# Kernel optimization log

Measured on AMD Instinct MI355X. Metric: run time of the kernel, lower is better.

Reference implementation:

```python
import jax, jax.numpy as jnp
import numpy as np

S, B, D_IN, D_OUT, E, R = 2048, 8, 1024, 4096, 8, 16

def setup_inputs() -> dict:
    key = jax.random.key(0)
    ks = jax.random.split(key, 6)
    x = jax.random.normal(ks[0], (S, B, D_IN), dtype=jnp.float32)
    gate_w = jax.random.normal(ks[1], (E, D_IN), dtype=jnp.float32) * 0.01  # std=0.01 init
    gate_b = jnp.zeros((E,), dtype=jnp.float32)  # init_lambda = 0
    W = jax.random.normal(ks[2], (D_OUT, D_IN), dtype=jnp.float32) * 0.02
    bias = jax.random.normal(ks[3], (D_OUT,), dtype=jnp.float32) * 0.02
    lora_A = jax.random.normal(ks[4], (E, R, D_IN), dtype=jnp.float32) * 0.02
    lora_B = jax.random.normal(ks[5], (E, D_OUT, R), dtype=jnp.float32) * 0.02
    return {"x": x, "gate_w": gate_w, "gate_b": gate_b, "W": W, "bias": bias,
            "lora_A": lora_A, "lora_B": lora_B}

def reference(x, gate_w, gate_b, W, bias, lora_A, lora_B):
    # gate: Linear(hidden, E) applied tokenwise, then mean over seq dim (dim 0, batch_first=False)
    gates = jnp.einsum('sbd,ed->sbe', x, gate_w) + gate_b      # [S,B,E]
    gate_weights = gates.mean(axis=0)                           # [B,E]
    # per-expert LoRA delta (detached in the torch original)
    delta = jnp.einsum('eor,eri->eoi', lora_B, lora_A)          # [E,D_OUT,D_IN]
    delta = jax.lax.stop_gradient(delta)
    # per-sample merged weight: W + sum_e g[b,e] * delta[e]
    W_b = W[None] + jnp.einsum('be,eoi->boi', gate_weights, delta)  # [B,D_OUT,D_IN]
    # per-sample linear (equivalent to looping functional_call over samples)
    out = jnp.einsum('sbi,boi->sbo', x, W_b) + bias             # [S,B,D_OUT]
    return out
```

## Files before the change

### kernel.cpp

```cpp
#include <hip/hip_runtime.h>
#include <stdint.h>

typedef unsigned short u16;
typedef __bf16 bf16x8 __attribute__((ext_vector_type(8)));
typedef float  f32x4  __attribute__((ext_vector_type(4)));

#define SDIM 2048
#define BDIM 8
#define DIN  1024
#define DOUT 4096
#define EDIM 8
#define RDIM 16
#define KAUG 1152
#define MDIM (SDIM*BDIM)
#define SCH  32
#define NT2  18

__device__ __forceinline__ u16 f2bf(float f) {
    __bf16 h = (__bf16)f;
    return __builtin_bit_cast(u16, h);
}

__device__ __forceinline__ void gload16(const u16* g, u16* lds) {
    __builtin_amdgcn_global_load_lds(
        (const __attribute__((address_space(1))) void*)g,
        (__attribute__((address_space(3))) void*)lds, 16, 0, 0);
}

#define VMCNT(n)  asm volatile("s_waitcnt vmcnt(" #n ")" ::: "memory")
#define LGKM0()   asm volatile("s_waitcnt lgkmcnt(0)" ::: "memory")
#define BARF()    do { asm volatile("" ::: "memory");                \
                       __builtin_amdgcn_s_barrier();                 \
                       asm volatile("" ::: "memory"); } while (0)

__global__ __launch_bounds__(256) void k1_reduce_convert(
    const float* __restrict__ x, u16* __restrict__ Xb, float* __restrict__ P)
{
    const int b  = blockIdx.x;
    const int sc = blockIdx.y;
    const int i  = threadIdx.x * 4;
    float a0 = 0.f, a1 = 0.f, a2 = 0.f, a3 = 0.f;
    const int s0 = sc * (SDIM / SCH);
    for (int s = s0; s < s0 + (SDIM / SCH); ++s) {
        const float4 v = *reinterpret_cast<const float4*>(
            &x[((size_t)s * BDIM + b) * DIN + i]);
        a0 += v.x; a1 += v.y; a2 += v.z; a3 += v.w;
        ushort4 u{f2bf(v.x), f2bf(v.y), f2bf(v.z), f2bf(v.w)};
        *reinterpret_cast<ushort4*>(&Xb[((size_t)s * BDIM + b) * KAUG + i]) = u;
    }
    float4 p{a0, a1, a2, a3};
    *reinterpret_cast<float4*>(&P[((size_t)sc * BDIM + b) * DIN + i]) = p;
}

__global__ __launch_bounds__(256) void k2_gates(
    const float* __restrict__ P, const float* __restrict__ gw,
    const float* __restrict__ gb, float* __restrict__ g)
{
    const int e = blockIdx.x, b = blockIdx.y, t = threadIdx.x;
    float dot = 0.f;
    for (int i = t; i < DIN; i += 256) {
        float xs = 0.f;
        #pragma unroll
        for (int c = 0; c < SCH; ++c) xs += P[((size_t)c * BDIM + b) * DIN + i];
        dot += xs * gw[(size_t)e * DIN + i];
    }
    __shared__ float red[256];
    red[t] = dot;
    __syncthreads();
    #pragma unroll
    for (int off = 128; off > 0; off >>= 1) {
        if (t < off) red[t] += red[t + off];
        __syncthreads();
    }
    if (t == 0) g[b * EDIM + e] = red[0] * (1.0f / SDIM) + gb[e];
}

__global__ __launch_bounds__(256) void kw_build_waug(
    const float* __restrict__ W, const float* __restrict__ lb, u16* __restrict__ Waug)
{
    const int o = blockIdx.x, t = threadIdx.x;
    for (int i = t; i < DIN; i += 256)
        Waug[(size_t)o * KAUG + i] = f2bf(W[(size_t)o * DIN + i]);
    if (t < EDIM * RDIM) {
        const int e = t >> 4, r = t & 15;
        Waug[(size_t)o * KAUG + DIN + t] =
            f2bf(lb[((size_t)e * DOUT + o) * RDIM + r]);
    }
}

__global__ __launch_bounds__(256) void kl_convert(
    const float* __restrict__ la, u16* __restrict__ LAb)
{
    const int idx = blockIdx.x * 256 + threadIdx.x;
    if (idx < EDIM * RDIM * DIN) LAb[idx] = f2bf(la[idx]);
}

__global__ __launch_bounds__(256) void gemm_lora(
    const u16* __restrict__ A, const u16* __restrict__ B,
    const float* __restrict__ G, u16* __restrict__ Xb)
{
    __shared__ __align__(16) u16 As[128][64];
    __shared__ __align__(16) u16 Bs[128][64];

    const int tid  = threadIdx.x;
    const int lane = tid & 63;
    const int l15  = lane & 15;
    const int l4   = lane >> 4;
    const int sw   = lane & 7;
    const int wid  = tid >> 6;
    const int wr   = wid >> 1;
    const int wc   = wid & 1;
    const int m0 = blockIdx.y * 128;

    f32x4 acc[4][4] = {};

    for (int kt = 0; kt < DIN / 64; ++kt) {
        #pragma unroll
        for (int ii = 0; ii < 4; ++ii) {
            const int cix = ii * 256 + tid;
            const int row = cix >> 3, cl = cix & 7;
            const int kof = kt * 64 + ((cl ^ (row & 7)) << 3);
            gload16(A + (size_t)(m0 + row) * KAUG + kof, &As[0][0] + cix * 8);
            gload16(B + (size_t)row * DIN + kof, &Bs[0][0] + cix * 8);
        }
        __syncthreads();
        #pragma unroll
        for (int ks = 0; ks < 2; ++ks) {
            bf16x8 av[4], bv[4];
            #pragma unroll
            for (int mi = 0; mi < 4; ++mi)
                av[mi] = *reinterpret_cast<const bf16x8*>(
                    &As[wr * 64 + mi * 16 + l15][((ks * 4 + l4) ^ sw) << 3]);
            #pragma unroll
            for (int ni = 0; ni < 4; ++ni)
                bv[ni] = *reinterpret_cast<const bf16x8*>(
                    &Bs[wc * 64 + ni * 16 + l15][((ks * 4 + l4) ^ sw) << 3]);
            #pragma unroll
            for (int mi = 0; mi < 4; ++mi)
                #pragma unroll
                for (int ni = 0; ni < 4; ++ni)
                    acc[mi][ni] = __builtin_amdgcn_mfma_f32_16x16x32_bf16(
                        av[mi], bv[ni], acc[mi][ni], 0, 0, 0);
        }
        __syncthreads();
    }

    #pragma unroll
    for (int mi = 0; mi < 4; ++mi) {
        const int r0 = m0 + wr * 64 + mi * 16 + l4 * 4;
        #pragma unroll
        for (int ni = 0; ni < 4; ++ni) {
            const int col = wc * 64 + ni * 16 + l15;
            const int e   = col >> 4;
            #pragma unroll
            for (int r = 0; r < 4; ++r) {
                const int row = r0 + r;
                const float gv = G[((row & 7) << 3) + e];
                Xb[(size_t)row * KAUG + DIN + col] = f2bf(gv * acc[mi][ni][r]);
            }
        }
    }
}

__global__ __launch_bounds__(512) void gemm_main(
    const u16* __restrict__ A, const u16* __restrict__ Bm,
    float* __restrict__ C, const float* __restrict__ bias)
{
    __shared__ __align__(16) u16 As[2][2][128][64];
    __shared__ __align__(16) u16 Bs[2][2][128][64];

    const int tid  = threadIdx.x;
    const int lane = tid & 63;
    const int l15  = lane & 15;
    const int l4   = lane >> 4;
    const int sw   = lane & 7;
    const int wid  = tid >> 6;
    const int wm   = wid >> 2;
    const int wn   = wid & 3;
    const int bh   = wn >> 1;
    const int bl   = wn & 1;

    const int f   = blockIdx.x + blockIdx.y * gridDim.x;
    const int xcd = f & 7, k = f >> 3;
    const int gn  = xcd & 3, gm = xcd >> 2;
    const int n0  = (gn * 4 + (k & 3)) * 256;
    const int m0  = (gm * 32 + (k >> 2)) * 256;

    f32x4  acc[8][4] = {};
    bf16x8 aq[2][2], bv[4][2];

    auto stageA = [&](int t, int hf) {
        const int buf = t & 1;
        #pragma unroll
        for (int ii = 0; ii < 2; ++ii) {
            const int cix = ii * 512 + tid;
            const int row = cix >> 3, cl = cix & 7;
            const int kof = t * 64 + ((cl ^ (row & 7)) << 3);
            gload16(A + (size_t)(m0 + hf * 128 + row) * KAUG + kof,
                    &As[buf][hf][0][0] + cix * 8);
        }
    };
    auto stageB = [&](int t, int hf) {
        const int buf = t & 1;
        #pragma unroll
        for (int ii = 0; ii < 2; ++ii) {
            const int cix = ii * 512 + tid;
            const int row = cix >> 3, cl = cix & 7;
            const int kof = t * 64 + ((cl ^ (row & 7)) << 3);
            gload16(Bm + (size_t)(n0 + hf * 128 + row) * KAUG + kof,
                    &Bs[buf][hf][0][0] + cix * 8);
        }
    };

    #define RD_BV(BUF)                                                        \
        _Pragma("unroll") for (int nf = 0; nf < 4; ++nf)                      \
            _Pragma("unroll") for (int kk = 0; kk < 2; ++kk)                  \
                bv[nf][kk] = *reinterpret_cast<const bf16x8*>(                \
                    &Bs[BUF][bh][bl * 64 + nf * 16 + l15]                     \
                       [((kk * 4 + l4) ^ sw) << 3]);
    #define RD_AQ(BUF, Q)                                                     \
        _Pragma("unroll") for (int fr = 0; fr < 2; ++fr)                      \
            _Pragma("unroll") for (int kk = 0; kk < 2; ++kk)                  \
                aq[fr][kk] = *reinterpret_cast<const bf16x8*>(                \
                    &As[BUF][wm][(Q) * 32 + fr * 16 + l15]                    \
                       [((kk * 4 + l4) ^ sw) << 3]);
    #define MMA(Q)                                                            \
        do {                                                                  \
            __builtin_amdgcn_s_setprio(1);                                    \
            _Pragma("unroll") for (int kk = 0; kk < 2; ++kk)                  \
                _Pragma("unroll") for (int fr = 0; fr < 2; ++fr)              \
                    _Pragma("unroll") for (int nf = 0; nf < 4; ++nf)          \
                        acc[(Q) * 2 + fr][nf] =                               \
                            __builtin_amdgcn_mfma_f32_16x16x32_bf16(          \
                                aq[fr][kk], bv[nf][kk],                       \
                                acc[(Q) * 2 + fr][nf], 0, 0, 0);              \
            __builtin_amdgcn_s_setprio(0);                                    \
        } while (0)

    stageA(0, 0); stageA(0, 1); stageB(0, 0); stageB(0, 1);
    stageA(1, 0); stageA(1, 1); stageB(1, 0); stageB(1, 1);
    VMCNT(8);
    BARF();

    for (int j = 0; j < NT2; ++j) {
        const int buf = j & 1;
        RD_BV(buf);
        RD_AQ(buf, 0);
        if (j >= 1 && j + 1 < NT2) stageA(j + 1, 0);
        BARF();
        LGKM0();
        __builtin_amdgcn_sched_barrier(0);
        MMA(0);
        BARF();
        RD_AQ(buf, 1);
        if (j >= 1 && j + 1 < NT2) stageA(j + 1, 1);
        BARF();
        LGKM0();
        __builtin_amdgcn_sched_barrier(0);
        MMA(1);
        BARF();
        RD_AQ(buf, 2);
        if (j + 2 < NT2) stageB(j + 2, 0);
        BARF();
        LGKM0();
        __builtin_amdgcn_sched_barrier(0);
        MMA(2);
        BARF();
        RD_AQ(buf, 3);
        if (j + 2 < NT2) stageB(j + 2, 1);
        BARF();
        LGKM0();
        __builtin_amdgcn_sched_barrier(0);
        MMA(3);
        if (j <= NT2 - 3) { VMCNT(4); } else { VMCNT(0); }
        BARF();
    }
    #undef RD_BV
    #undef RD_AQ
    #undef MMA

    #pragma unroll
    for (int a = 0; a < 8; ++a) {
        const int row0 = m0 + wm * 128 + a * 16 + l4 * 4;
        #pragma unroll
        for (int nf = 0; nf < 4; ++nf) {
            const int col = n0 + wn * 64 + nf * 16 + l15;
            const float badd = bias[col];
            float* cp = C + (size_t)row0 * DOUT + col;
            #pragma unroll
            for (int q = 0; q < 4; ++q)
                cp[(size_t)q * DOUT] = acc[a][nf][q] + badd;
        }
    }
}

extern "C" void kernel_launch(void* const* d_in, const int* in_sizes, int n_in,
                              void* d_out, int out_size, void* d_ws, size_t ws_size,
                              hipStream_t stream)
{
    const float* x    = (const float*)d_in[0];
    const float* gw   = (const float*)d_in[1];
    const float* gb   = (const float*)d_in[2];
    const float* W    = (const float*)d_in[3];
    const float* bias = (const float*)d_in[4];
    const float* la   = (const float*)d_in[5];
    const float* lb   = (const float*)d_in[6];
    float* out = (float*)d_out;

    char* ws = (char*)d_ws;
    u16*   Xb   = (u16*)(ws);
    u16*   Waug = (u16*)(ws + 37748736);
    float* P    = (float*)(ws + 47185920);
    u16*   LAb  = (u16*)(ws + 48234496);
    float* G    = (float*)(ws + 48496640);

    k1_reduce_convert<<<dim3(BDIM, SCH), 256, 0, stream>>>(x, Xb, P);
    kw_build_waug<<<DOUT, 256, 0, stream>>>(W, lb, Waug);
    kl_convert<<<(EDIM * RDIM * DIN + 255) / 256, 256, 0, stream>>>(la, LAb);
    k2_gates<<<dim3(EDIM, BDIM), 256, 0, stream>>>(P, gw, gb, G);
    gemm_lora<<<dim3(1, MDIM / 128), 256, 0, stream>>>(Xb, LAb, G, Xb);
    gemm_main<<<dim3(DOUT / 256, MDIM / 256), 512, 0, stream>>>(
        Xb, Waug, out, bias);
}
```

Measured before the change: 249.0 us.

## Pre-swizzle weights into MFMA fragment layout and load B directly to registers

The augmented weight matrix is now built in a fragment-major layout, so each lane's 16-byte B operand for the 16x16x32 MFMA is one contiguous global load. The main GEMM drops the B shared-memory tile and reads B straight into two register banks that alternate between even and odd K tiles, which also halves the per-tile barrier count. The aim is to cut LDS traffic and synchronisation for B. In exchange every wave reads B from global/L2 with no reuse across the block, register pressure rises, and each tile ends with a full vmcnt(0) wait, leaving no prefetch depth beyond one tile.

```diff
diff --git a/kernel.cpp b/kernel.cpp
--- a/kernel.cpp
+++ b/kernel.cpp
@@ -15,6 +15,8 @@
 #define MDIM (SDIM*BDIM)
 #define SCH  32
 #define NT2  18
+#define NCB  (DOUT/16)
+#define NKC  (KAUG/8)
 
 __device__ __forceinline__ u16 f2bf(float f) {
     __bf16 h = (__bf16)f;
@@ -28,7 +30,6 @@
 }
 
 #define VMCNT(n)  asm volatile("s_waitcnt vmcnt(" #n ")" ::: "memory")
-#define LGKM0()   asm volatile("s_waitcnt lgkmcnt(0)" ::: "memory")
 #define BARF()    do { asm volatile("" ::: "memory");                \
                        __builtin_amdgcn_s_barrier();                 \
                        asm volatile("" ::: "memory"); } while (0)
@@ -75,16 +76,29 @@
     if (t == 0) g[b * EDIM + e] = red[0] * (1.0f / SDIM) + gb[e];
 }
 
-__global__ __launch_bounds__(256) void kw_build_waug(
-    const float* __restrict__ W, const float* __restrict__ lb, u16* __restrict__ Waug)
-{
-    const int o = blockIdx.x, t = threadIdx.x;
-    for (int i = t; i < DIN; i += 256)
-        Waug[(size_t)o * KAUG + i] = f2bf(W[(size_t)o * DIN + i]);
-    if (t < EDIM * RDIM) {
-        const int e = t >> 4, r = t & 15;
-        Waug[(size_t)o * KAUG + DIN + t] =
-            f2bf(lb[((size_t)e * DOUT + o) * RDIM + r]);
+__global__ __launch_bounds__(256) void kwf_build_waugf(
+    const float* __restrict__ W, const float* __restrict__ lb, u16* __restrict__ WF)
+{
+    const int cb = blockIdx.x, t = threadIdx.x;
+    const int ln = t & 15;
+    const int o  = cb * 16 + ln;
+    #pragma unroll
+    for (int bq = 0; bq < 9; ++bq) {
+        const int kc = (t >> 4) + 16 * bq;
+        u16 v[8];
+        if (kc < 128) {
+            #pragma unroll
+            for (int q = 0; q < 8; ++q)
+                v[q] = f2bf(W[(size_t)o * DIN + kc * 8 + q]);
+        } else {
+            const int e = (kc - 128) >> 1, rh = (kc - 128) & 1;
+            #pragma unroll
+            for (int q = 0; q < 8; ++q)
+                v[q] = f2bf(lb[((size_t)e * DOUT + o) * RDIM + rh * 8 + q]);
+        }
+        u16* dst = WF + (((size_t)cb * NKC + kc) * 16 + ln) * 8;
+        *reinterpret_cast<ushort4*>(dst)     = ushort4{v[0], v[1], v[2], v[3]};
+        *reinterpret_cast<ushort4*>(dst + 4) = ushort4{v[4], v[5], v[6], v[7]};
     }
 }
 
@@ -163,11 +177,10 @@
 }
 
 __global__ __launch_bounds__(512) void gemm_main(
-    const u16* __restrict__ A, const u16* __restrict__ Bm,
+    const u16* __restrict__ A, const u16* __restrict__ WF,
     float* __restrict__ C, const float* __restrict__ bias)
 {
     __shared__ __align__(16) u16 As[2][2][128][64];
-    __shared__ __align__(16) u16 Bs[2][2][128][64];
 
     const int tid  = threadIdx.x;
     const int lane = tid & 63;
@@ -177,17 +190,18 @@
     const int wid  = tid >> 6;
     const int wm   = wid >> 2;
     const int wn   = wid & 3;
-    const int bh   = wn >> 1;
-    const int bl   = wn & 1;
 
     const int f   = blockIdx.x + blockIdx.y * gridDim.x;
-    const int xcd = f & 7, k = f >> 3;
+    const int xcd = f & 7, kk_ = f >> 3;
     const int gn  = xcd & 3, gm = xcd >> 2;
-    const int n0  = (gn * 4 + (k & 3)) * 256;
-    const int m0  = (gm * 32 + (k >> 2)) * 256;
+    const int n0  = (gn * 4 + (kk_ & 3)) * 256;
+    const int m0  = (gm * 32 + (kk_ >> 2)) * 256;
+
+    const int cb0 = (n0 >> 4) + wn * 4;
 
     f32x4  acc[8][4] = {};
-    bf16x8 aq[2][2], bv[4][2];
+    bf16x8 aq[2][2];
+    bf16x8 bvE[4][2], bvO[4][2];
 
     auto stageA = [&](int t, int hf) {
         const int buf = t & 1;
@@ -200,31 +214,19 @@
                     &As[buf][hf][0][0] + cix * 8);
         }
     };
-    auto stageB = [&](int t, int hf) {
-        const int buf = t & 1;
-        #pragma unroll
-        for (int ii = 0; ii < 2; ++ii) {
-            const int cix = ii * 512 + tid;
-            const int row = cix >> 3, cl = cix & 7;
-            const int kof = t * 64 + ((cl ^ (row & 7)) << 3);
-            gload16(Bm + (size_t)(n0 + hf * 128 + row) * KAUG + kof,
-                    &Bs[buf][hf][0][0] + cix * 8);
-        }
-    };
-
-    #define RD_BV(BUF)                                                        \
+
+    #define BLOAD(T, KK, BANK)                                                \
         _Pragma("unroll") for (int nf = 0; nf < 4; ++nf)                      \
-            _Pragma("unroll") for (int kk = 0; kk < 2; ++kk)                  \
-                bv[nf][kk] = *reinterpret_cast<const bf16x8*>(                \
-                    &Bs[BUF][bh][bl * 64 + nf * 16 + l15]                     \
-                       [((kk * 4 + l4) ^ sw) << 3]);
+            BANK[nf][KK] = *reinterpret_cast<const bf16x8*>(                  \
+                WF + (((size_t)(cb0 + nf) * NKC + ((T) * 8 + (KK) * 4 + l4))  \
+                      * 16 + l15) * 8);
     #define RD_AQ(BUF, Q)                                                     \
         _Pragma("unroll") for (int fr = 0; fr < 2; ++fr)                      \
             _Pragma("unroll") for (int kk = 0; kk < 2; ++kk)                  \
                 aq[fr][kk] = *reinterpret_cast<const bf16x8*>(                \
                     &As[BUF][wm][(Q) * 32 + fr * 16 + l15]                    \
                        [((kk * 4 + l4) ^ sw) << 3]);
-    #define MMA(Q)                                                            \
+    #define MMA(Q, BANK)                                                      \
         do {                                                                  \
             __builtin_amdgcn_s_setprio(1);                                    \
             _Pragma("unroll") for (int kk = 0; kk < 2; ++kk)                  \
@@ -232,52 +234,44 @@
                     _Pragma("unroll") for (int nf = 0; nf < 4; ++nf)          \
                         acc[(Q) * 2 + fr][nf] =                               \
                             __builtin_amdgcn_mfma_f32_16x16x32_bf16(          \
-                                aq[fr][kk], bv[nf][kk],                       \
+                                aq[fr][kk], BANK[nf][kk],                     \
                                 acc[(Q) * 2 + fr][nf], 0, 0, 0);              \
             __builtin_amdgcn_s_setprio(0);                                    \
         } while (0)
 
-    stageA(0, 0); stageA(0, 1); stageB(0, 0); stageB(0, 1);
-    stageA(1, 0); stageA(1, 1); stageB(1, 0); stageB(1, 1);
-    VMCNT(8);
+    #define TILE(T, BVU, BVL)                                                 \
+    do {                                                                      \
+        const int buf_ = (T) & 1;                                             \
+                                             \
+        RD_AQ(buf_, 0);                                                       \
+        if ((T) + 1 < NT2) { stageA((T) + 1, 0); BLOAD((T) + 1, 0, BVL); }    \
+        MMA(0, BVU);                                                          \
+        RD_AQ(buf_, 1);                                                       \
+        MMA(1, BVU);                                                          \
+        BARF();                                                               \
+                                             \
+        RD_AQ(buf_, 2);                                                       \
+        if ((T) + 1 < NT2) { stageA((T) + 1, 1); BLOAD((T) + 1, 1, BVL); }    \
+        MMA(2, BVU);                                                          \
+        RD_AQ(buf_, 3);                                                       \
+        MMA(3, BVU);                                                          \
+        VMCNT(0);                                                             \
+        BARF();                                                               \
+    } while (0)
+
+    stageA(0, 0); stageA(0, 1);
+    BLOAD(0, 0, bvE); BLOAD(0, 1, bvE);
+    VMCNT(0);
     BARF();
 
-    for (int j = 0; j < NT2; ++j) {
-        const int buf = j & 1;
-        RD_BV(buf);
-        RD_AQ(buf, 0);
-        if (j >= 1 && j + 1 < NT2) stageA(j + 1, 0);
-        BARF();
-        LGKM0();
-        __builtin_amdgcn_sched_barrier(0);
-        MMA(0);
-        BARF();
-        RD_AQ(buf, 1);
-        if (j >= 1 && j + 1 < NT2) stageA(j + 1, 1);
-        BARF();
-        LGKM0();
-        __builtin_amdgcn_sched_barrier(0);
-        MMA(1);
-        BARF();
-        RD_AQ(buf, 2);
-        if (j + 2 < NT2) stageB(j + 2, 0);
-        BARF();
-        LGKM0();
-        __builtin_amdgcn_sched_barrier(0);
-        MMA(2);
-        BARF();
-        RD_AQ(buf, 3);
-        if (j + 2 < NT2) stageB(j + 2, 1);
-        BARF();
-        LGKM0();
-        __builtin_amdgcn_sched_barrier(0);
-        MMA(3);
-        if (j <= NT2 - 3) { VMCNT(4); } else { VMCNT(0); }
-        BARF();
-    }
-    #undef RD_BV
+    for (int jj = 0; jj < NT2; jj += 2) {
+        TILE(jj,     bvE, bvO);
+        TILE(jj + 1, bvO, bvE);
+    }
+    #undef TILE
+    #undef MMA
     #undef RD_AQ
-    #undef MMA
+    #undef BLOAD
 
     #pragma unroll
     for (int a = 0; a < 8; ++a) {
@@ -309,16 +303,16 @@
 
     char* ws = (char*)d_ws;
     u16*   Xb   = (u16*)(ws);
-    u16*   Waug = (u16*)(ws + 37748736);
+    u16*   WF   = (u16*)(ws + 37748736);
     float* P    = (float*)(ws + 47185920);
     u16*   LAb  = (u16*)(ws + 48234496);
     float* G    = (float*)(ws + 48496640);
 
     k1_reduce_convert<<<dim3(BDIM, SCH), 256, 0, stream>>>(x, Xb, P);
-    kw_build_waug<<<DOUT, 256, 0, stream>>>(W, lb, Waug);
+    kwf_build_waugf<<<NCB, 256, 0, stream>>>(W, lb, WF);
     kl_convert<<<(EDIM * RDIM * DIN + 255) / 256, 256, 0, stream>>>(la, LAb);
     k2_gates<<<dim3(EDIM, BDIM), 256, 0, stream>>>(P, gw, gb, G);
     gemm_lora<<<dim3(1, MDIM / 128), 256, 0, stream>>>(Xb, LAb, G, Xb);
     gemm_main<<<dim3(DOUT / 256, MDIM / 256), 512, 0, stream>>>(
-        Xb, Waug, out, bias);
-}
+        Xb, WF, out, bias);
+}
```

Result: no change. 251.5 us (+1.0%).
